# Performance work log

Measured on AMD Instinct MI355X. Metric: run time of the kernel, lower is better.

## Reference

```python
import jax, jax.numpy as jnp
import numpy as np

B, T, D = 16, 1024, 384
T_OUT = 4096  # fixed expanded length (mean duration 4 frames/token)


def setup_inputs() -> dict:
    key = jax.random.key(0)
    k_x, k_ids, k_noise = jax.random.split(key, 3)
    x = jax.random.normal(k_x, (B, T, D), dtype=jnp.float32)
    # Build integer durations that sum to exactly T_OUT per row by counting
    # T_OUT sorted segment assignments into T buckets.
    ids = jnp.sort(jax.random.randint(k_ids, (B, T_OUT), 0, T), axis=1)
    counts = jax.vmap(lambda r: jnp.zeros((T,), jnp.float32).at[r].add(1.0))(ids)
    # Add noise in (-0.4, 0.4) so floor(dur + 0.5) recovers counts but the
    # rounding path in the module is exercised with non-integer inputs.
    noise = jax.random.uniform(k_noise, (B, T), minval=-0.4, maxval=0.4)
    dur = counts + noise
    return {"x": x, "dur": dur, "out_len": T_OUT}


def reference(x, dur, out_len):
    # dur[dur < 0] = 0
    dur = jnp.maximum(dur, 0.0)
    # (dur + 0.5).long() -> truncation == floor for non-negative values
    counts = jnp.floor(dur + 0.5).astype(jnp.int32)  # [B, T]
    # repeat_interleave as a gather: output position j maps to the token i
    # whose cumulative-count interval contains j.
    csum = jnp.cumsum(counts, axis=1)                 # [B, T]
    pos = jnp.arange(out_len, dtype=jnp.int32)        # [T_out]
    idx = jax.vmap(lambda c: jnp.searchsorted(c, pos, side="right"))(csum)  # [B, T_out]
    idx = jnp.clip(idx, 0, x.shape[1] - 1)
    out = jnp.take_along_axis(x, idx[:, :, None], axis=1)  # [B, T_out, D]
    return out
```

## Files before the change

kernel.cpp:

```cpp
#include <hip/hip_runtime.h>
#include <hip/hip_bf16.h>


#define LR_B     16
#define LR_T     1024
#define LR_D4    96
#define LR_TOUT  4096
#define LR_CHUNK 16
#define LR_NCH   (LR_T / LR_CHUNK)
#define LR_NTHR  384

__device__ __forceinline__ int lr_count(float d) {
    return (int)floorf(fmaxf(d, 0.0f) + 0.5f);
}

__global__ __launch_bounds__(LR_NTHR) void lr_fused(
    const float* __restrict__ dur, const float4* __restrict__ x,
    float4* __restrict__ out) {
    const int blk  = blockIdx.x;
    const int b    = blk >> 6;
    const int c    = blk & (LR_NCH - 1);
    const int t0   = c * LR_CHUNK;
    const int tid  = threadIdx.x;
    const int lane = tid & 63;
    const int wid  = tid >> 6;

    const float* drow = dur + b * LR_T;

    int sum = 0;
    #pragma unroll
    for (int k = 0; k < 3; ++k) {
        int j = tid + k * LR_NTHR;
        if (j < t0) sum += lr_count(drow[j]);
    }
    #pragma unroll
    for (int off = 1; off < 64; off <<= 1)
        sum += __shfl_xor(sum, off, 64);

    __shared__ int wsum[LR_NTHR / 64];
    __shared__ int cs[LR_CHUNK + 1];
    if (lane == 0) wsum[wid] = sum;
    __syncthreads();

    if (wid == 0) {
        int base = 0;
        #pragma unroll
        for (int w = 0; w < LR_NTHR / 64; ++w) base += wsum[w];
        if (lane < LR_CHUNK) {
            int v = lr_count(drow[t0 + lane]);
            #pragma unroll
            for (int off = 1; off < LR_CHUNK; off <<= 1) {
                int u = __shfl_up(v, off, 64);
                if (lane >= off) v += u;
            }
            cs[lane + 1] = base + v;
            if (lane == 0) cs[0] = base;
        }
    }
    __syncthreads();

    const int g = tid / LR_D4;
    const int d = tid - g * LR_D4;
    const float4* xrow = x + (size_t)(b * LR_T + t0) * LR_D4 + d;
    float4* orow = out + (size_t)b * LR_TOUT * LR_D4 + d;

    #pragma unroll
    for (int i = 0; i < LR_CHUNK; ++i) {
        int s = min(cs[i], LR_TOUT);
        int e = min(cs[i + 1], LR_TOUT);
        if (c == LR_NCH - 1 && i == LR_CHUNK - 1) e = LR_TOUT;
        const float4 v = xrow[i * LR_D4];
        for (int p = s + g; p < e; p += 4)
            orow[(size_t)p * LR_D4] = v;
    }
}

extern "C" void kernel_launch(void* const* d_in, const int* in_sizes, int n_in,
                              void* d_out, int out_size, void* d_ws, size_t ws_size,
                              hipStream_t stream) {
    const float* x   = (const float*)d_in[0];
    const float* dur = (const float*)d_in[1];

    lr_fused<<<LR_B * LR_NCH, LR_NTHR, 0, stream>>>(
        dur, (const float4*)x, (float4*)d_out);
}
```

Before: 26.11 us.

## Partition work by output windows with per-block scan and binary-search gather

Switches from input-token chunks that scatter variable-length runs to fixed 64-row output windows. Each block scans the full duration row into shared memory, binary-searches the source token for each output row, then gathers rows with nontemporal stores. This balances store work evenly across blocks and makes stores contiguous, avoiding the uneven per-token loops. The cost is a redundant full-row scan in every block and re-reading of x rows that repeat.

```diff
diff --git a/kernel.cpp b/kernel.cpp
--- a/kernel.cpp
+++ b/kernel.cpp
@@ -6,72 +6,80 @@
 #define LR_T     1024
 #define LR_D4    96
 #define LR_TOUT  4096
-#define LR_CHUNK 16
-#define LR_NCH   (LR_T / LR_CHUNK)
+#define LR_WIN   64
+#define LR_NWIN  (LR_TOUT / LR_WIN)
 #define LR_NTHR  384
+
+typedef float lr_f4 __attribute__((ext_vector_type(4)));
 
 __device__ __forceinline__ int lr_count(float d) {
     return (int)floorf(fmaxf(d, 0.0f) + 0.5f);
 }
 
 __global__ __launch_bounds__(LR_NTHR) void lr_fused(
-    const float* __restrict__ dur, const float4* __restrict__ x,
-    float4* __restrict__ out) {
+    const float* __restrict__ dur, const lr_f4* __restrict__ x,
+    lr_f4* __restrict__ out) {
     const int blk  = blockIdx.x;
     const int b    = blk >> 6;
-    const int c    = blk & (LR_NCH - 1);
-    const int t0   = c * LR_CHUNK;
+    const int w    = blk & (LR_NWIN - 1);
+    const int o0   = w * LR_WIN;
     const int tid  = threadIdx.x;
     const int lane = tid & 63;
     const int wid  = tid >> 6;
 
-    const float* drow = dur + b * LR_T;
+    __shared__ int cs[LR_T];
+    __shared__ int tok[LR_WIN];
+    __shared__ int wbase[4];
 
-    int sum = 0;
+    const lr_f4* drow4 = (const lr_f4*)(dur + b * LR_T);
+    int c0 = 0, c1 = 0, c2 = 0, c3 = 0, s = 0;
+    if (tid < LR_T / 4) {
+        lr_f4 dv = drow4[tid];
+        c0 = lr_count(dv.x);
+        c1 = c0 + lr_count(dv.y);
+        c2 = c1 + lr_count(dv.z);
+        c3 = c2 + lr_count(dv.w);
+        s = c3;
+    }
+    int v = s;
     #pragma unroll
-    for (int k = 0; k < 3; ++k) {
-        int j = tid + k * LR_NTHR;
-        if (j < t0) sum += lr_count(drow[j]);
+    for (int off = 1; off < 64; off <<= 1) {
+        int u = __shfl_up(v, off, 64);
+        if (lane >= off) v += u;
     }
-    #pragma unroll
-    for (int off = 1; off < 64; off <<= 1)
-        sum += __shfl_xor(sum, off, 64);
-
-    __shared__ int wsum[LR_NTHR / 64];
-    __shared__ int cs[LR_CHUNK + 1];
-    if (lane == 0) wsum[wid] = sum;
+    if (tid < LR_T / 4 && lane == 63) wbase[wid] = v;
+    __syncthreads();
+    if (tid < LR_T / 4) {
+        int base = v - s;
+        #pragma unroll
+        for (int ww = 0; ww < 4; ++ww)
+            if (ww < wid) base += wbase[ww];
+        int4 cw = make_int4(base + c0, base + c1, base + c2, base + c3);
+        *(int4*)&cs[tid * 4] = cw;
+    }
     __syncthreads();
 
-    if (wid == 0) {
-        int base = 0;
-        #pragma unroll
-        for (int w = 0; w < LR_NTHR / 64; ++w) base += wsum[w];
-        if (lane < LR_CHUNK) {
-            int v = lr_count(drow[t0 + lane]);
-            #pragma unroll
-            for (int off = 1; off < LR_CHUNK; off <<= 1) {
-                int u = __shfl_up(v, off, 64);
-                if (lane >= off) v += u;
-            }
-            cs[lane + 1] = base + v;
-            if (lane == 0) cs[0] = base;
+    if (tid < LR_WIN) {
+        const int j = o0 + tid;
+        int lo = 0, hi = LR_T;
+        while (lo < hi) {
+            int mid = (lo + hi) >> 1;
+            if (cs[mid] <= j) lo = mid + 1; else hi = mid;
         }
+        tok[tid] = min(lo, LR_T - 1);
     }
     __syncthreads();
 
     const int g = tid / LR_D4;
     const int d = tid - g * LR_D4;
-    const float4* xrow = x + (size_t)(b * LR_T + t0) * LR_D4 + d;
-    float4* orow = out + (size_t)b * LR_TOUT * LR_D4 + d;
+    const lr_f4* xb = x + (size_t)b * LR_T * LR_D4 + d;
+    lr_f4* ob = out + ((size_t)b * LR_TOUT + o0 + g) * LR_D4 + d;
 
     #pragma unroll
-    for (int i = 0; i < LR_CHUNK; ++i) {
-        int s = min(cs[i], LR_TOUT);
-        int e = min(cs[i + 1], LR_TOUT);
-        if (c == LR_NCH - 1 && i == LR_CHUNK - 1) e = LR_TOUT;
-        const float4 v = xrow[i * LR_D4];
-        for (int p = s + g; p < e; p += 4)
-            orow[(size_t)p * LR_D4] = v;
+    for (int it = 0; it < LR_WIN / 4; ++it) {
+        const int t = tok[it * 4 + g];
+        lr_f4 val = xb[(size_t)t * LR_D4];
+        __builtin_nontemporal_store(val, &ob[(size_t)it * 4 * LR_D4]);
     }
 }
 
@@ -81,6 +89,6 @@
     const float* x   = (const float*)d_in[0];
     const float* dur = (const float*)d_in[1];
 
-    lr_fused<<<LR_B * LR_NCH, LR_NTHR, 0, stream>>>(
-        dur, (const float4*)x, (float4*)d_out);
+    lr_fused<<<LR_B * LR_NWIN, LR_NTHR, 0, stream>>>(
+        dur, (const lr_f4*)x, (lr_f4*)d_out);
 }
```

After: 24.65 us. -5.6%, faster.
